# Optimization experiments

Hardware: AMD Instinct MI355X
Metric: run time of the kernel (lower is better)

## Reference

```python
import jax, jax.numpy as jnp
import numpy as np

T, D, E, INTER, TOP_K = 512, 1024, 64, 512, 4


def setup_inputs() -> dict:
    key = jax.random.key(0)
    k1, k2, k3, k4, k5 = jax.random.split(key, 5)
    s = 1.0 / np.sqrt(D)
    return {
        "hidden_states": jax.random.normal(k1, (T, D), dtype=jnp.float32),
        "gate_w": jax.random.normal(k2, (E, D), dtype=jnp.float32) * s,      # MoEGate.weight
        "w_gate": jax.random.normal(k3, (E, INTER, D), dtype=jnp.float32) * s,  # gate_proj per expert
        "w_up": jax.random.normal(k4, (E, INTER, D), dtype=jnp.float32) * s,    # up_proj per expert
        "w_down": jax.random.normal(k5, (E, D, INTER), dtype=jnp.float32) * (1.0 / np.sqrt(INTER)),  # down_proj
    }


def _moe_forward(x, gate_w, w_gate, w_up, w_down):
    # Router: logits -> softmax -> top-k -> renormalize (Qwen path of select_experts)
    logits = x @ gate_w.T                                  # [T, E]
    probs = jax.nn.softmax(logits, axis=-1)
    topk_w, topk_ids = jax.lax.top_k(probs, TOP_K)          # [T, K]
    topk_w = topk_w / jnp.sum(topk_w, axis=-1, keepdims=True)  # renormalize (norm_topk_prob)
    # Combine weights as sparse [T, E] matrix (identity logical->physical mapping)
    t_idx = jnp.arange(x.shape[0])[:, None]
    combine = jnp.zeros((x.shape[0], gate_w.shape[0]), dtype=x.dtype).at[t_idx, topk_ids].add(topk_w)
    # Expert FFN (SwiGLU), dense-over-experts reference for grouped GEMM dispatch
    g = jnp.einsum("td,efd->etf", x, w_gate)               # [E, T, INTER]
    u = jnp.einsum("td,efd->etf", x, w_up)
    h = jax.nn.silu(g) * u
    y = jnp.einsum("etf,edf->etd", h, w_down)              # [E, T, D]
    out = jnp.einsum("te,etd->td", combine, y)             # weighted combine
    return out


def reference(hidden_states, gate_w, w_gate, w_up, w_down):
    return _moe_forward(hidden_states, gate_w, w_gate, w_up, w_down)
```

## Files before the change

### kernel.cpp

```cpp
#include <hip/hip_runtime.h>
#include <cstddef>

#define T_TOK 512
#define D_DIM 1024
#define E_EXP 64
#define INTER 512
#define TOPK 4

typedef __bf16 bf16x8 __attribute__((ext_vector_type(8)));
typedef __bf16 bf16x4 __attribute__((ext_vector_type(4)));
typedef float f32x4 __attribute__((ext_vector_type(4)));

__device__ __forceinline__ void async16(float4* ldsdst, const void* g) {
  __builtin_amdgcn_global_load_lds(
      (const __attribute__((address_space(1))) void*)g,
      (__attribute__((address_space(3))) void*)ldsdst, 16, 0, 0);
}

__device__ __forceinline__ void cvt_split8(const float4 a, const float4 b,
                                           bf16x8& h, bf16x8& l) {
  float f[8] = {a.x, a.y, a.z, a.w, b.x, b.y, b.z, b.w};
#pragma unroll
  for (int i = 0; i < 8; i++) {
    const __bf16 hv = (__bf16)f[i];
    h[i] = hv;
    l[i] = (__bf16)(f[i] - (float)hv);
  }
}

__global__ __launch_bounds__(64) void router_kernel(
    const float* __restrict__ x, const float* __restrict__ gate_w,
    int* __restrict__ cnt, int* __restrict__ list, float* __restrict__ pairw,
    __bf16* __restrict__ x_hi, __bf16* __restrict__ x_lo) {
  const int t = blockIdx.x;
  const int e = threadIdx.x;
  const float4* xr = (const float4*)(x + (size_t)t * D_DIM);
  const float4* gr = (const float4*)(gate_w + (size_t)e * D_DIM);
  float acc = 0.f;
#pragma unroll 8
  for (int i = 0; i < D_DIM / 4; i++) {
    float4 a = xr[i], b = gr[i];
    acc += a.x * b.x + a.y * b.y + a.z * b.z + a.w * b.w;
  }
  {
    bf16x8 h0, l0, h1, l1;
    cvt_split8(xr[e * 4 + 0], xr[e * 4 + 1], h0, l0);
    cvt_split8(xr[e * 4 + 2], xr[e * 4 + 3], h1, l1);
    __bf16* xh = x_hi + (size_t)t * D_DIM + e * 16;
    __bf16* xl = x_lo + (size_t)t * D_DIM + e * 16;
    *(bf16x8*)(xh) = h0; *(bf16x8*)(xh + 8) = h1;
    *(bf16x8*)(xl) = l0; *(bf16x8*)(xl + 8) = l1;
  }
  float m = acc;
  for (int off = 32; off; off >>= 1) m = fmaxf(m, __shfl_xor(m, off, 64));
  float p = __expf(acc - m);
  float s = p;
  for (int off = 32; off; off >>= 1) s += __shfl_xor(s, off, 64);
  float prob = p / s;

  float val = prob;
  int ids[TOPK];
  float ws[TOPK];
  float wsum = 0.f;
#pragma unroll
  for (int k = 0; k < TOPK; k++) {
    float v = val;
    int idx = e;
    for (int off = 32; off; off >>= 1) {
      float ov = __shfl_xor(v, off, 64);
      int oi = __shfl_xor(idx, off, 64);
      if (ov > v || (ov == v && oi < idx)) { v = ov; idx = oi; }
    }
    ids[k] = idx;
    ws[k] = v;
    wsum += v;
    if (e == idx) val = -1.f;
  }
  if (e < TOPK) {
    const int k = e;
    const int ex = ids[k];
    const float w = ws[k] / wsum;
    const int p_id = t * TOPK + k;
    pairw[p_id] = w;
    const int pos = atomicAdd(&cnt[ex], 1);
    list[ex * T_TOK + pos] = p_id;
  }
}

#define BF1 32
#define BT1 64
#define NK1 (D_DIM / 64)
__global__ __launch_bounds__(256) void stage1_kernel(
    const __bf16* __restrict__ x_hi, const __bf16* __restrict__ x_lo,
    const float* __restrict__ w_gate, const float* __restrict__ w_up,
    const int* __restrict__ cnt, const int* __restrict__ list,
    const float* __restrict__ pairw,
    __bf16* __restrict__ h_hi, __bf16* __restrict__ h_lo) {
  const int e = blockIdx.x;
  const int fbase = blockIdx.y * BF1;
  const int n = cnt[e];
  if (n == 0) return;
  __shared__ float4 lds[2][2048];
  const int tid = threadIdx.x;
  const int w = tid >> 6;
  const int lane = tid & 63;
  const int lrow = lane & 15;
  const int lk = lane >> 4;
  const int* mylist = list + e * T_TOK;

  const int wrow = tid >> 3;
  const int wblk = tid & 7;
  const float* gsrc = w_gate + ((size_t)e * INTER + fbase + wrow) * D_DIM + wblk * 8;
  const float* usrc = w_up + ((size_t)e * INTER + fbase + wrow) * D_DIM + wblk * 8;
  const int wunit = wrow * 8 + (wblk ^ (wrow & 7));

  float4 wreg[4];

  for (int tb = 0; tb < n; tb += BT1) {
    const __bf16* xsrc[4];
#pragma unroll
    for (int r = 0; r < 4; r++) {
      const int u = w * 256 + r * 64 + lane;
      const int uu = u & 511;
      const int row = uu >> 3;
      const int blk = (uu & 7) ^ (row & 7);
      const int slot = tb + row;
      const int pid = mylist[slot < n ? slot : 0];
      const __bf16* base = (u < 512) ? x_hi : x_lo;
      xsrc[r] = base + (size_t)(pid >> 2) * D_DIM + blk * 8;
    }

    auto stage_load = [&](int buf, int kb) {
      const float4* g4 = (const float4*)(gsrc + kb);
      const float4* u4 = (const float4*)(usrc + kb);
      wreg[0] = g4[0]; wreg[1] = g4[1];
      wreg[2] = u4[0]; wreg[3] = u4[1];
      float4* B = &lds[buf][0];
#pragma unroll
      for (int r = 0; r < 4; r++)
        async16(B + 1024 + w * 256 + r * 64, xsrc[r] + kb);
    };
    auto convert_write = [&](int buf) {
      __bf16* L = (__bf16*)&lds[buf][0];
      bf16x8 h0, l0;
      cvt_split8(wreg[0], wreg[1], h0, l0);
      *(bf16x8*)(L + (size_t)wunit * 8) = h0;
      *(bf16x8*)(L + (size_t)(wunit + 256) * 8) = l0;
      cvt_split8(wreg[2], wreg[3], h0, l0);
      *(bf16x8*)(L + (size_t)(wunit + 512) * 8) = h0;
      *(bf16x8*)(L + (size_t)(wunit + 768) * 8) = l0;
    };

    f32x4 accg[2] = {};
    f32x4 accu[2] = {};
    const bool active = (tb + w * 16) < n;

    stage_load(0, 0);
    convert_write(0);
    for (int ki = 0; ki < NK1; ki++) {
      __syncthreads();
      if (ki + 1 < NK1) stage_load((ki + 1) & 1, (ki + 1) * 64);
      if (active) {
        const __bf16* L = (const __bf16*)&lds[ki & 1][0];
#pragma unroll
        for (int s = 0; s < 2; s++) {
          const int blk = s * 4 + lk;
          const int xr = w * 16 + lrow;
          const int xu = xr * 8 + (blk ^ (xr & 7));
          const bf16x8 xh = *(const bf16x8*)(L + (size_t)(1024 + xu) * 8);
          const bf16x8 xl = *(const bf16x8*)(L + (size_t)(1536 + xu) * 8);
#pragma unroll
          for (int i = 0; i < 2; i++) {
            const int fr = i * 16 + lrow;
            const int fu = fr * 8 + (blk ^ (fr & 7));
            const bf16x8 gh = *(const bf16x8*)(L + (size_t)fu * 8);
            const bf16x8 gl = *(const bf16x8*)(L + (size_t)(256 + fu) * 8);
            const bf16x8 uh = *(const bf16x8*)(L + (size_t)(512 + fu) * 8);
            const bf16x8 ul = *(const bf16x8*)(L + (size_t)(768 + fu) * 8);
            accg[i] = __builtin_amdgcn_mfma_f32_16x16x32_bf16(gh, xh, accg[i], 0, 0, 0);
            accg[i] = __builtin_amdgcn_mfma_f32_16x16x32_bf16(gh, xl, accg[i], 0, 0, 0);
            accg[i] = __builtin_amdgcn_mfma_f32_16x16x32_bf16(gl, xh, accg[i], 0, 0, 0);
            accu[i] = __builtin_amdgcn_mfma_f32_16x16x32_bf16(uh, xh, accu[i], 0, 0, 0);
            accu[i] = __builtin_amdgcn_mfma_f32_16x16x32_bf16(uh, xl, accu[i], 0, 0, 0);
            accu[i] = __builtin_amdgcn_mfma_f32_16x16x32_bf16(ul, xh, accu[i], 0, 0, 0);
          }
        }
      }
      if (ki + 1 < NK1) convert_write((ki + 1) & 1);
    }
    const int slot = tb + w * 16 + lrow;
    if (slot < n) {
      const int pid = mylist[slot];
      const float wp = pairw[pid];
      __bf16* hh = h_hi + (size_t)pid * INTER + fbase;
      __bf16* hl = h_lo + (size_t)pid * INTER + fbase;
#pragma unroll
      for (int i = 0; i < 2; i++) {
        bf16x4 vh, vl;
#pragma unroll
        for (int r = 0; r < 4; r++) {
          const float g = accg[i][r];
          const float u = accu[i][r];
          const float v = wp * (g / (1.f + __expf(-g))) * u;
          const __bf16 hv = (__bf16)v;
          vh[r] = hv;
          vl[r] = (__bf16)(v - (float)hv);
        }
        *(bf16x4*)(hh + i * 16 + lk * 4) = vh;
        *(bf16x4*)(hl + i * 16 + lk * 4) = vl;
      }
    }
  }
}

#define BF2 64
#define NK2 (INTER / 64)
__global__ __launch_bounds__(256) void stage2_kernel(
    const float* __restrict__ w_down, const int* __restrict__ cnt,
    const int* __restrict__ list, const __bf16* __restrict__ h_hi,
    const __bf16* __restrict__ h_lo, float* __restrict__ out) {
  const int e = blockIdx.x;
  const int dbase = blockIdx.y * BF2;
  const int n = cnt[e];
  if (n == 0) return;
  __shared__ float4 lds[2][2048];
  const int tid = threadIdx.x;
  const int w = tid >> 6;
  const int lane = tid & 63;
  const int lrow = lane & 15;
  const int lk = lane >> 4;
  const int* mylist = list + e * T_TOK;

  const int wrow = tid >> 3;
  const int wblk = tid & 7;
  const float* dsrc0 = w_down + ((size_t)e * D_DIM + dbase + wrow) * INTER + wblk * 8;
  const float* dsrc1 = w_down + ((size_t)e * D_DIM + dbase + wrow + 32) * INTER + wblk * 8;
  const int wunit0 = wrow * 8 + (wblk ^ (wrow & 7));
  const int wunit1 = wunit0 + 256;

  float4 wreg[4];

  for (int tb = 0; tb < n; tb += BT1) {
    const __bf16* hsrc[4];
#pragma unroll
    for (int r = 0; r < 4; r++) {
      const int u = w * 256 + r * 64 + lane;
      const int uu = u & 511;
      const int row = uu >> 3;
      const int blk = (uu & 7) ^ (row & 7);
      const int slot = tb + row;
      const int pid = mylist[slot < n ? slot : 0];
      const __bf16* base = (u < 512) ? h_hi : h_lo;
      hsrc[r] = base + (size_t)pid * INTER + blk * 8;
    }

    auto stage_load = [&](int buf, int kb) {
      const float4* a4 = (const float4*)(dsrc0 + kb);
      const float4* b4 = (const float4*)(dsrc1 + kb);
      wreg[0] = a4[0]; wreg[1] = a4[1];
      wreg[2] = b4[0]; wreg[3] = b4[1];
      float4* B = &lds[buf][0];
#pragma unroll
      for (int r = 0; r < 4; r++)
        async16(B + 1024 + w * 256 + r * 64, hsrc[r] + kb);
    };
    auto convert_write = [&](int buf) {
      __bf16* L = (__bf16*)&lds[buf][0];
      bf16x8 h0, l0;
      cvt_split8(wreg[0], wreg[1], h0, l0);
      *(bf16x8*)(L + (size_t)wunit0 * 8) = h0;
      *(bf16x8*)(L + (size_t)(wunit0 + 512) * 8) = l0;
      cvt_split8(wreg[2], wreg[3], h0, l0);
      *(bf16x8*)(L + (size_t)wunit1 * 8) = h0;
      *(bf16x8*)(L + (size_t)(wunit1 + 512) * 8) = l0;
    };

    f32x4 acc[4] = {};
    const bool active = (tb + w * 16) < n;

    stage_load(0, 0);
    convert_write(0);
    for (int ki = 0; ki < NK2; ki++) {
      __syncthreads();
      if (ki + 1 < NK2) stage_load((ki + 1) & 1, (ki + 1) * 64);
      if (active) {
        const __bf16* L = (const __bf16*)&lds[ki & 1][0];
#pragma unroll
        for (int s = 0; s < 2; s++) {
          const int blk = s * 4 + lk;
          const int hr = w * 16 + lrow;
          const int hu = hr * 8 + (blk ^ (hr & 7));
          const bf16x8 hh = *(const bf16x8*)(L + (size_t)(1024 + hu) * 8);
          const bf16x8 hl = *(const bf16x8*)(L + (size_t)(1536 + hu) * 8);
#pragma unroll
          for (int i = 0; i < 4; i++) {
            const int dr = i * 16 + lrow;
            const int du = dr * 8 + (blk ^ (dr & 7));
            const bf16x8 wh = *(const bf16x8*)(L + (size_t)du * 8);
            const bf16x8 wl = *(const bf16x8*)(L + (size_t)(512 + du) * 8);
            acc[i] = __builtin_amdgcn_mfma_f32_16x16x32_bf16(wh, hh, acc[i], 0, 0, 0);
            acc[i] = __builtin_amdgcn_mfma_f32_16x16x32_bf16(wh, hl, acc[i], 0, 0, 0);
            acc[i] = __builtin_amdgcn_mfma_f32_16x16x32_bf16(wl, hh, acc[i], 0, 0, 0);
          }
        }
      }
      if (ki + 1 < NK2) convert_write((ki + 1) & 1);
    }
    const int slot = tb + w * 16 + lrow;
    if (slot < n) {
      const int tok = mylist[slot] >> 2;
      float* op = out + (size_t)tok * D_DIM + dbase;
#pragma unroll
      for (int i = 0; i < 4; i++) {
#pragma unroll
        for (int r = 0; r < 4; r++)
          atomicAdd(&op[i * 16 + lk * 4 + r], acc[i][r]);
      }
    }
  }
}

extern "C" void kernel_launch(void* const* d_in, const int* in_sizes, int n_in,
                              void* d_out, int out_size, void* d_ws, size_t ws_size,
                              hipStream_t stream) {
  const float* x = (const float*)d_in[0];
  const float* gate_w = (const float*)d_in[1];
  const float* w_gate = (const float*)d_in[2];
  const float* w_up = (const float*)d_in[3];
  const float* w_down = (const float*)d_in[4];
  float* out = (float*)d_out;

  char* ws = (char*)d_ws;
  size_t off = 0;
  int* cnt = (int*)(ws + off); off += 256;
  int* list = (int*)(ws + off); off += (size_t)E_EXP * T_TOK * 4;
  float* pairw = (float*)(ws + off); off += (size_t)T_TOK * TOPK * 4;
  __bf16* h_hi = (__bf16*)(ws + off); off += (size_t)T_TOK * TOPK * INTER * 2;
  __bf16* h_lo = (__bf16*)(ws + off); off += (size_t)T_TOK * TOPK * INTER * 2;
  __bf16* x_hi = (__bf16*)(ws + off); off += (size_t)T_TOK * D_DIM * 2;
  __bf16* x_lo = (__bf16*)(ws + off); off += (size_t)T_TOK * D_DIM * 2;

  hipMemsetAsync(cnt, 0, E_EXP * sizeof(int), stream);
  hipMemsetAsync(out, 0, (size_t)T_TOK * D_DIM * sizeof(float), stream);

  router_kernel<<<T_TOK, 64, 0, stream>>>(x, gate_w, cnt, list, pairw, x_hi, x_lo);
  stage1_kernel<<<dim3(E_EXP, INTER / BF1), 256, 0, stream>>>(
      x_hi, x_lo, w_gate, w_up, cnt, list, pairw, h_hi, h_lo);
  stage2_kernel<<<dim3(E_EXP, D_DIM / BF2), 256, 0, stream>>>(
      w_down, cnt, list, h_hi, h_lo, out);
}
```

Before: 455.4 us.

## Load activation fragments directly into registers and double-buffer weight tiles

Both expert GEMM stages now load the token activation fragments (x or h hi/lo) straight from global memory into registers in MFMA layout, instead of staging them through LDS with async global-to-LDS copies. This halves the LDS footprint per buffer. The K loop is unrolled by two with separate register sets for weights and activations, so the next tile's loads overlap with compute. The low part of h is stored scaled by 256 and rescaled through a separate accumulator in stage 2, which keeps more precision in the bf16 residual. The cost is more registers and less coalesced per-lane global reads of activations.

Result: faster. 437.7 us (-3.9%).

```diff
diff --git a/kernel.cpp b/kernel.cpp
--- a/kernel.cpp
+++ b/kernel.cpp
@@ -10,12 +10,6 @@
 typedef __bf16 bf16x8 __attribute__((ext_vector_type(8)));
 typedef __bf16 bf16x4 __attribute__((ext_vector_type(4)));
 typedef float f32x4 __attribute__((ext_vector_type(4)));
-
-__device__ __forceinline__ void async16(float4* ldsdst, const void* g) {
-  __builtin_amdgcn_global_load_lds(
-      (const __attribute__((address_space(1))) void*)g,
-      (__attribute__((address_space(3))) void*)ldsdst, 16, 0, 0);
-}
 
 __device__ __forceinline__ void cvt_split8(const float4 a, const float4 b,
                                            bf16x8& h, bf16x8& l) {
@@ -100,7 +94,7 @@
   const int fbase = blockIdx.y * BF1;
   const int n = cnt[e];
   if (n == 0) return;
-  __shared__ float4 lds[2][2048];
+  __shared__ bf16x8 lds[2][1024];
   const int tid = threadIdx.x;
   const int w = tid >> 6;
   const int lane = tid & 63;
@@ -114,86 +108,88 @@
   const float* usrc = w_up + ((size_t)e * INTER + fbase + wrow) * D_DIM + wblk * 8;
   const int wunit = wrow * 8 + (wblk ^ (wrow & 7));
 
-  float4 wreg[4];
+  float4 wA[4], wB[4];
+  bf16x8 xA[4], xB[4];
 
   for (int tb = 0; tb < n; tb += BT1) {
-    const __bf16* xsrc[4];
-#pragma unroll
-    for (int r = 0; r < 4; r++) {
-      const int u = w * 256 + r * 64 + lane;
-      const int uu = u & 511;
-      const int row = uu >> 3;
-      const int blk = (uu & 7) ^ (row & 7);
-      const int slot = tb + row;
-      const int pid = mylist[slot < n ? slot : 0];
-      const __bf16* base = (u < 512) ? x_hi : x_lo;
-      xsrc[r] = base + (size_t)(pid >> 2) * D_DIM + blk * 8;
-    }
-
-    auto stage_load = [&](int buf, int kb) {
-      const float4* g4 = (const float4*)(gsrc + kb);
-      const float4* u4 = (const float4*)(usrc + kb);
-      wreg[0] = g4[0]; wreg[1] = g4[1];
-      wreg[2] = u4[0]; wreg[3] = u4[1];
-      float4* B = &lds[buf][0];
-#pragma unroll
-      for (int r = 0; r < 4; r++)
-        async16(B + 1024 + w * 256 + r * 64, xsrc[r] + kb);
-    };
-    auto convert_write = [&](int buf) {
-      __bf16* L = (__bf16*)&lds[buf][0];
+    const bool active = (tb + w * 16) < n;
+    const int slot1 = tb + w * 16 + lrow;
+    const int pidx = mylist[(slot1 < n) ? slot1 : 0];
+    const __bf16* xbh = x_hi + (size_t)(pidx >> 2) * D_DIM + lk * 8;
+    const __bf16* xbl = x_lo + (size_t)(pidx >> 2) * D_DIM + lk * 8;
+
+    auto LOADW = [&](float4* r, int kt) {
+      const float4* g4 = (const float4*)(gsrc + kt * 64);
+      const float4* u4 = (const float4*)(usrc + kt * 64);
+      r[0] = g4[0]; r[1] = g4[1]; r[2] = u4[0]; r[3] = u4[1];
+    };
+    auto LOADX = [&](bf16x8* r, int kt) {
+      r[0] = *(const bf16x8*)(xbh + kt * 64);
+      r[1] = *(const bf16x8*)(xbl + kt * 64);
+      r[2] = *(const bf16x8*)(xbh + kt * 64 + 32);
+      r[3] = *(const bf16x8*)(xbl + kt * 64 + 32);
+    };
+    auto CVTW = [&](const float4* r, int buf) {
       bf16x8 h0, l0;
-      cvt_split8(wreg[0], wreg[1], h0, l0);
-      *(bf16x8*)(L + (size_t)wunit * 8) = h0;
-      *(bf16x8*)(L + (size_t)(wunit + 256) * 8) = l0;
-      cvt_split8(wreg[2], wreg[3], h0, l0);
-      *(bf16x8*)(L + (size_t)(wunit + 512) * 8) = h0;
-      *(bf16x8*)(L + (size_t)(wunit + 768) * 8) = l0;
+      cvt_split8(r[0], r[1], h0, l0);
+      lds[buf][wunit] = h0;
+      lds[buf][wunit + 256] = l0;
+      cvt_split8(r[2], r[3], h0, l0);
+      lds[buf][wunit + 512] = h0;
+      lds[buf][wunit + 768] = l0;
     };
 
     f32x4 accg[2] = {};
     f32x4 accu[2] = {};
-    const bool active = (tb + w * 16) < n;
-
-    stage_load(0, 0);
-    convert_write(0);
-    for (int ki = 0; ki < NK1; ki++) {
-      __syncthreads();
-      if (ki + 1 < NK1) stage_load((ki + 1) & 1, (ki + 1) * 64);
-      if (active) {
-        const __bf16* L = (const __bf16*)&lds[ki & 1][0];
-#pragma unroll
-        for (int s = 0; s < 2; s++) {
-          const int blk = s * 4 + lk;
-          const int xr = w * 16 + lrow;
-          const int xu = xr * 8 + (blk ^ (xr & 7));
-          const bf16x8 xh = *(const bf16x8*)(L + (size_t)(1024 + xu) * 8);
-          const bf16x8 xl = *(const bf16x8*)(L + (size_t)(1536 + xu) * 8);
-#pragma unroll
-          for (int i = 0; i < 2; i++) {
-            const int fr = i * 16 + lrow;
-            const int fu = fr * 8 + (blk ^ (fr & 7));
-            const bf16x8 gh = *(const bf16x8*)(L + (size_t)fu * 8);
-            const bf16x8 gl = *(const bf16x8*)(L + (size_t)(256 + fu) * 8);
-            const bf16x8 uh = *(const bf16x8*)(L + (size_t)(512 + fu) * 8);
-            const bf16x8 ul = *(const bf16x8*)(L + (size_t)(768 + fu) * 8);
-            accg[i] = __builtin_amdgcn_mfma_f32_16x16x32_bf16(gh, xh, accg[i], 0, 0, 0);
-            accg[i] = __builtin_amdgcn_mfma_f32_16x16x32_bf16(gh, xl, accg[i], 0, 0, 0);
-            accg[i] = __builtin_amdgcn_mfma_f32_16x16x32_bf16(gl, xh, accg[i], 0, 0, 0);
-            accu[i] = __builtin_amdgcn_mfma_f32_16x16x32_bf16(uh, xh, accu[i], 0, 0, 0);
-            accu[i] = __builtin_amdgcn_mfma_f32_16x16x32_bf16(uh, xl, accu[i], 0, 0, 0);
-            accu[i] = __builtin_amdgcn_mfma_f32_16x16x32_bf16(ul, xh, accu[i], 0, 0, 0);
-          }
+
+    auto COMPUTE = [&](int buf, const bf16x8* xr) {
+      if (!active) return;
+      const bf16x8* U = &lds[buf][0];
+#pragma unroll
+      for (int s = 0; s < 2; s++) {
+        const bf16x8 xh = xr[s * 2];
+        const bf16x8 xl = xr[s * 2 + 1];
+        const int blk = s * 4 + lk;
+#pragma unroll
+        for (int i = 0; i < 2; i++) {
+          const int fr = i * 16 + lrow;
+          const int fu = fr * 8 + (blk ^ (fr & 7));
+          const bf16x8 gh = U[fu];
+          const bf16x8 gl = U[fu + 256];
+          const bf16x8 uh = U[fu + 512];
+          const bf16x8 ul = U[fu + 768];
+          accg[i] = __builtin_amdgcn_mfma_f32_16x16x32_bf16(gh, xh, accg[i], 0, 0, 0);
+          accg[i] = __builtin_amdgcn_mfma_f32_16x16x32_bf16(gh, xl, accg[i], 0, 0, 0);
+          accg[i] = __builtin_amdgcn_mfma_f32_16x16x32_bf16(gl, xh, accg[i], 0, 0, 0);
+          accu[i] = __builtin_amdgcn_mfma_f32_16x16x32_bf16(uh, xh, accu[i], 0, 0, 0);
+          accu[i] = __builtin_amdgcn_mfma_f32_16x16x32_bf16(uh, xl, accu[i], 0, 0, 0);
+          accu[i] = __builtin_amdgcn_mfma_f32_16x16x32_bf16(ul, xh, accu[i], 0, 0, 0);
         }
       }
-      if (ki + 1 < NK1) convert_write((ki + 1) & 1);
-    }
-    const int slot = tb + w * 16 + lrow;
-    if (slot < n) {
-      const int pid = mylist[slot];
-      const float wp = pairw[pid];
-      __bf16* hh = h_hi + (size_t)pid * INTER + fbase;
-      __bf16* hl = h_lo + (size_t)pid * INTER + fbase;
+    };
+
+    LOADW(wA, 0);
+    LOADW(wB, 1);
+    if (active) LOADX(xA, 0);
+    CVTW(wA, 0);
+    if (active) LOADX(xB, 1);
+
+    for (int ki = 0; ki < NK1; ki += 2) {
+      __syncthreads();
+      if (ki + 2 < NK1) LOADW(wA, ki + 2);
+      COMPUTE(0, xA);
+      CVTW(wB, 1);
+      if (active && ki + 2 < NK1) LOADX(xA, ki + 2);
+      __syncthreads();
+      if (ki + 3 < NK1) LOADW(wB, ki + 3);
+      COMPUTE(1, xB);
+      if (ki + 2 < NK1) CVTW(wA, 0);
+      if (active && ki + 3 < NK1) LOADX(xB, ki + 3);
+    }
+    if (slot1 < n) {
+      const float wp = pairw[pidx];
+      __bf16* hh = h_hi + (size_t)pidx * INTER + fbase;
+      __bf16* hl = h_lo + (size_t)pidx * INTER + fbase;
 #pragma unroll
       for (int i = 0; i < 2; i++) {
         bf16x4 vh, vl;
@@ -204,7 +200,7 @@
           const float v = wp * (g / (1.f + __expf(-g))) * u;
           const __bf16 hv = (__bf16)v;
           vh[r] = hv;
-          vl[r] = (__bf16)(v - (float)hv);
+          vl[r] = (__bf16)((v - (float)hv) * 256.f);
         }
         *(bf16x4*)(hh + i * 16 + lk * 4) = vh;
         *(bf16x4*)(hl + i * 16 + lk * 4) = vl;
@@ -214,6 +210,7 @@
 }
 
 #define BF2 64
+#define BT2 64
 #define NK2 (INTER / 64)
 __global__ __launch_bounds__(256) void stage2_kernel(
     const float* __restrict__ w_down, const int* __restrict__ cnt,
@@ -223,7 +220,7 @@
   const int dbase = blockIdx.y * BF2;
   const int n = cnt[e];
   if (n == 0) return;
-  __shared__ float4 lds[2][2048];
+  __shared__ bf16x8 lds[2][1024];
   const int tid = threadIdx.x;
   const int w = tid >> 6;
   const int lane = tid & 63;
@@ -234,87 +231,91 @@
   const int wrow = tid >> 3;
   const int wblk = tid & 7;
   const float* dsrc0 = w_down + ((size_t)e * D_DIM + dbase + wrow) * INTER + wblk * 8;
-  const float* dsrc1 = w_down + ((size_t)e * D_DIM + dbase + wrow + 32) * INTER + wblk * 8;
+  const float* dsrc1 = dsrc0 + (size_t)32 * INTER;
   const int wunit0 = wrow * 8 + (wblk ^ (wrow & 7));
   const int wunit1 = wunit0 + 256;
 
-  float4 wreg[4];
-
-  for (int tb = 0; tb < n; tb += BT1) {
-    const __bf16* hsrc[4];
-#pragma unroll
-    for (int r = 0; r < 4; r++) {
-      const int u = w * 256 + r * 64 + lane;
-      const int uu = u & 511;
-      const int row = uu >> 3;
-      const int blk = (uu & 7) ^ (row & 7);
-      const int slot = tb + row;
-      const int pid = mylist[slot < n ? slot : 0];
-      const __bf16* base = (u < 512) ? h_hi : h_lo;
-      hsrc[r] = base + (size_t)pid * INTER + blk * 8;
-    }
-
-    auto stage_load = [&](int buf, int kb) {
-      const float4* a4 = (const float4*)(dsrc0 + kb);
-      const float4* b4 = (const float4*)(dsrc1 + kb);
-      wreg[0] = a4[0]; wreg[1] = a4[1];
-      wreg[2] = b4[0]; wreg[3] = b4[1];
-      float4* B = &lds[buf][0];
-#pragma unroll
-      for (int r = 0; r < 4; r++)
-        async16(B + 1024 + w * 256 + r * 64, hsrc[r] + kb);
-    };
-    auto convert_write = [&](int buf) {
-      __bf16* L = (__bf16*)&lds[buf][0];
+  float4 wA[4], wB[4];
+  bf16x8 hA[4], hB[4];
+
+  for (int tb = 0; tb < n; tb += BT2) {
+    const bool active = (tb + w * 16) < n;
+    const int slot1 = tb + w * 16 + lrow;
+    const int pidx = mylist[(slot1 < n) ? slot1 : 0];
+    const __bf16* hbh = h_hi + (size_t)pidx * INTER + lk * 8;
+    const __bf16* hbl = h_lo + (size_t)pidx * INTER + lk * 8;
+
+    auto LOADW = [&](float4* r, int kt) {
+      const float4* a4 = (const float4*)(dsrc0 + kt * 64);
+      const float4* b4 = (const float4*)(dsrc1 + kt * 64);
+      r[0] = a4[0]; r[1] = a4[1]; r[2] = b4[0]; r[3] = b4[1];
+    };
+    auto LOADH = [&](bf16x8* r, int kt) {
+      r[0] = *(const bf16x8*)(hbh + kt * 64);
+      r[1] = *(const bf16x8*)(hbl + kt * 64);
+      r[2] = *(const bf16x8*)(hbh + kt * 64 + 32);
+      r[3] = *(const bf16x8*)(hbl + kt * 64 + 32);
+    };
+    auto CVTW = [&](const float4* r, int buf) {
       bf16x8 h0, l0;
-      cvt_split8(wreg[0], wreg[1], h0, l0);
-      *(bf16x8*)(L + (size_t)wunit0 * 8) = h0;
-      *(bf16x8*)(L + (size_t)(wunit0 + 512) * 8) = l0;
-      cvt_split8(wreg[2], wreg[3], h0, l0);
-      *(bf16x8*)(L + (size_t)wunit1 * 8) = h0;
-      *(bf16x8*)(L + (size_t)(wunit1 + 512) * 8) = l0;
+      cvt_split8(r[0], r[1], h0, l0);
+      lds[buf][wunit0] = h0;
+      lds[buf][wunit0 + 512] = l0;
+      cvt_split8(r[2], r[3], h0, l0);
+      lds[buf][wunit1] = h0;
+      lds[buf][wunit1 + 512] = l0;
     };
 
     f32x4 acc[4] = {};
-    const bool active = (tb + w * 16) < n;
-
-    stage_load(0, 0);
-    convert_write(0);
-    for (int ki = 0; ki < NK2; ki++) {
-      __syncthreads();
-      if (ki + 1 < NK2) stage_load((ki + 1) & 1, (ki + 1) * 64);
-      if (active) {
-        const __bf16* L = (const __bf16*)&lds[ki & 1][0];
-#pragma unroll
-        for (int s = 0; s < 2; s++) {
-          const int blk = s * 4 + lk;
-          const int hr = w * 16 + lrow;
-          const int hu = hr * 8 + (blk ^ (hr & 7));
-          const bf16x8 hh = *(const bf16x8*)(L + (size_t)(1024 + hu) * 8);
-          const bf16x8 hl = *(const bf16x8*)(L + (size_t)(1536 + hu) * 8);
-#pragma unroll
-          for (int i = 0; i < 4; i++) {
-            const int dr = i * 16 + lrow;
-            const int du = dr * 8 + (blk ^ (dr & 7));
-            const bf16x8 wh = *(const bf16x8*)(L + (size_t)du * 8);
-            const bf16x8 wl = *(const bf16x8*)(L + (size_t)(512 + du) * 8);
-            acc[i] = __builtin_amdgcn_mfma_f32_16x16x32_bf16(wh, hh, acc[i], 0, 0, 0);
-            acc[i] = __builtin_amdgcn_mfma_f32_16x16x32_bf16(wh, hl, acc[i], 0, 0, 0);
-            acc[i] = __builtin_amdgcn_mfma_f32_16x16x32_bf16(wl, hh, acc[i], 0, 0, 0);
-          }
+    f32x4 accb[4] = {};
+
+    auto COMPUTE = [&](int buf, const bf16x8* hr) {
+      if (!active) return;
+      const bf16x8* U = &lds[buf][0];
+#pragma unroll
+      for (int s = 0; s < 2; s++) {
+        const bf16x8 hh = hr[s * 2];
+        const bf16x8 hl = hr[s * 2 + 1];
+        const int blk = s * 4 + lk;
+#pragma unroll
+        for (int i = 0; i < 4; i++) {
+          const int dr = i * 16 + lrow;
+          const int du = dr * 8 + (blk ^ (dr & 7));
+          const bf16x8 wh = U[du];
+          const bf16x8 wl = U[du + 512];
+          acc[i] = __builtin_amdgcn_mfma_f32_16x16x32_bf16(wh, hh, acc[i], 0, 0, 0);
+          acc[i] = __builtin_amdgcn_mfma_f32_16x16x32_bf16(wl, hh, acc[i], 0, 0, 0);
+          accb[i] = __builtin_amdgcn_mfma_f32_16x16x32_bf16(wh, hl, accb[i], 0, 0, 0);
         }
       }
-      if (ki + 1 < NK2) convert_write((ki + 1) & 1);
-    }
-    const int slot = tb + w * 16 + lrow;
-    if (slot < n) {
-      const int tok = mylist[slot] >> 2;
+    };
+
+    LOADW(wA, 0);
+    LOADW(wB, 1);
+    if (active) LOADH(hA, 0);
+    CVTW(wA, 0);
+    if (active) LOADH(hB, 1);
+
+    for (int ki = 0; ki < NK2; ki += 2) {
+      __syncthreads();
+      if (ki + 2 < NK2) LOADW(wA, ki + 2);
+      COMPUTE(0, hA);
+      CVTW(wB, 1);
+      if (active && ki + 2 < NK2) LOADH(hA, ki + 2);
+      __syncthreads();
+      if (ki + 3 < NK2) LOADW(wB, ki + 3);
+      COMPUTE(1, hB);
+      if (ki + 2 < NK2) CVTW(wA, 0);
+      if (active && ki + 3 < NK2) LOADH(hB, ki + 3);
+    }
+    if (slot1 < n) {
+      const int tok = pidx >> 2;
       float* op = out + (size_t)tok * D_DIM + dbase;
 #pragma unroll
       for (int i = 0; i < 4; i++) {
 #pragma unroll
         for (int r = 0; r < 4; r++)
-          atomicAdd(&op[i * 16 + lk * 4 + r], acc[i][r]);
+          atomicAdd(&op[i * 16 + lk * 4 + r], acc[i][r] + accb[i][r] * 0.00390625f);
       }
     }
   }
```
